# Optimization experiments

Measured on AMD Instinct MI355X. Metric: run time of the kernel, lower is better.

## Reference

```python
import jax, jax.numpy as jnp
import numpy as np

N_NODES = 50000
N_EDGES = 800000
F_DIM = 128   # float_feat_dim
H_DIM = 64    # hidden_dim
NEG_SLOPE = 0.2


def setup_inputs() -> dict:
    key = jax.random.key(0)
    ks = jax.random.split(key, 12)
    in_dim = F_DIM + 1
    sc_in = 1.0 / np.sqrt(in_dim)
    sc_h = 1.0 / np.sqrt(H_DIM)
    return {
        "x_float": jax.random.normal(ks[0], (N_NODES, F_DIM), dtype=jnp.float32),
        "x_binary": jax.random.uniform(ks[1], (N_NODES,), dtype=jnp.float32),
        "edge_index": jax.random.randint(ks[2], (2, N_EDGES), 0, N_NODES, dtype=jnp.int64),
        "Wl": jax.random.normal(ks[3], (H_DIM, in_dim), dtype=jnp.float32) * sc_in,
        "bl": jnp.zeros((H_DIM,), dtype=jnp.float32),
        "Wr": jax.random.normal(ks[4], (H_DIM, in_dim), dtype=jnp.float32) * sc_in,
        "br": jnp.zeros((H_DIM,), dtype=jnp.float32),
        "att": jax.random.normal(ks[5], (H_DIM,), dtype=jnp.float32) * sc_h,
        "gat_bias": jnp.zeros((H_DIM,), dtype=jnp.float32),
        "Wo": jax.random.normal(ks[6], (F_DIM, H_DIM), dtype=jnp.float32) * sc_h,
        "bo": jnp.zeros((F_DIM,), dtype=jnp.float32),
        "dispersion": jnp.zeros((F_DIM,), dtype=jnp.float32),
    }


def reference(x_float, x_binary, edge_index, Wl, bl, Wr, br, att, gat_bias, Wo, bo, dispersion):
    N = x_float.shape[0]
    # concat float feats with binary feature -> [N, F+1]
    x = jnp.concatenate([x_float, x_binary[:, None]], axis=1)
    # add self loops (PyG GATv2Conv default)
    loops = jnp.arange(N, dtype=edge_index.dtype)
    src = jnp.concatenate([edge_index[0], loops])  # [E+N]
    dst = jnp.concatenate([edge_index[1], loops])
    # separate source/target linear projections (share_weights=False)
    xl = x @ Wl.T + bl  # [N, H]
    xr = x @ Wr.T + br  # [N, H]
    # per-edge GATv2 attention score: a^T LeakyReLU(x_l[j] + x_r[i])
    m = xl[src] + xr[dst]                      # [E+N, H]
    m = jnp.where(m > 0, m, NEG_SLOPE * m)
    e = m @ att                                # [E+N]
    # segment softmax over destination neighborhoods
    emax = jax.ops.segment_max(e, dst, num_segments=N)  # self loops => every seg nonempty
    ex = jnp.exp(e - emax[dst])
    denom = jax.ops.segment_sum(ex, dst, num_segments=N)
    alpha = ex / denom[dst]                    # [E+N]
    # weighted scatter-aggregate of source projections
    out = jax.ops.segment_sum(alpha[:, None] * xl[src], dst, num_segments=N) + gat_bias
    h = jax.nn.elu(out)                        # [N, H]
    logits = h @ Wo.T + bo                     # [N, F]
    return logits, jax.nn.softplus(dispersion)
```

## Files before the change

kernel.cpp:

```cpp
#include <hip/hip_runtime.h>
#include <hip/hip_bf16.h>
#include <math.h>

#define N_NODES 50000
#define N_EDGES 800000
#define F_DIM 128
#define H_DIM 64
#define IN_DIM 129
#define NPAD 50176
#define ETOT (N_EDGES + N_NODES)
#define PROJ_BLKS ((N_NODES + 63) / 64)
#define CNT_BLKS  ((N_EDGES + 255) / 256)

typedef __hip_bfloat16 bf16;
typedef __attribute__((ext_vector_type(8))) short bf16x8;
typedef __attribute__((ext_vector_type(4))) float f32x4;

static __device__ __forceinline__ float bs2f(short s) {
    union { float f; unsigned u; } c; c.u = ((unsigned)(unsigned short)s) << 16; return c.f;
}
static __device__ __forceinline__ short f2bs(float f) {
    union { bf16 b; short s; } u; u.b = __float2bfloat16(f); return u.s;
}

__global__ __launch_bounds__(256) void phase1_kernel(
    const float* __restrict__ xf, const float* __restrict__ xb,
    const float* __restrict__ Wl, const float* __restrict__ bl,
    const float* __restrict__ Wr, const float* __restrict__ br,
    const int* __restrict__ edst,
    bf16* __restrict__ xl, bf16* __restrict__ xr,
    int* __restrict__ cnt, int* __restrict__ rank)
{
    if (blockIdx.x >= PROJ_BLKS) {
        int e = (blockIdx.x - PROJ_BLKS) * 256 + threadIdx.x;
        if (e < N_EDGES) rank[e] = atomicAdd(&cnt[edst[e]], 1);
        return;
    }

    int wave = threadIdx.x >> 6;
    int lane = threadIdx.x & 63;
    int n = lane & 15, q = lane >> 4;
    int node0 = blockIdx.x * 64;

    bf16x8 bhi[2][4], blo[2][4];
    float biasv[2], w128[2];
    #pragma unroll
    for (int nt = 0; nt < 2; ++nt) {
        int ch = wave * 32 + nt * 16 + n;
        const float* wrow = (ch < 64) ? (Wl + (size_t)ch * IN_DIM)
                                      : (Wr + (size_t)(ch - 64) * IN_DIM);
        #pragma unroll
        for (int ks = 0; ks < 4; ++ks) {
            bf16x8 hi, lo;
            #pragma unroll
            for (int j = 0; j < 8; ++j) {
                float v = wrow[ks * 32 + q * 8 + j];
                short hs = f2bs(v);
                hi[j] = hs;
                lo[j] = f2bs(v - bs2f(hs));
            }
            bhi[nt][ks] = hi;
            blo[nt][ks] = lo;
        }
        biasv[nt] = (ch < 64) ? bl[ch] : br[ch - 64];
        w128[nt]  = wrow[128];
    }

    #pragma unroll
    for (int mt = 0; mt < 4; ++mt) {
        int nb = node0 + mt * 16;
        if (nb >= N_NODES) break;
        const float* xrow = xf + (size_t)(nb + n) * F_DIM;
        bf16x8 a[4];
        #pragma unroll
        for (int ks = 0; ks < 4; ++ks) {
            float4 u = *(const float4*)(xrow + ks * 32 + q * 8);
            float4 v = *(const float4*)(xrow + ks * 32 + q * 8 + 4);
            bf16x8 t;
            t[0] = f2bs(u.x); t[1] = f2bs(u.y); t[2] = f2bs(u.z); t[3] = f2bs(u.w);
            t[4] = f2bs(v.x); t[5] = f2bs(v.y); t[6] = f2bs(v.z); t[7] = f2bs(v.w);
            a[ks] = t;
        }
        f32x4 acc[2] = {{0.f,0.f,0.f,0.f},{0.f,0.f,0.f,0.f}};
        #pragma unroll
        for (int ks = 0; ks < 4; ++ks) {
            #pragma unroll
            for (int nt = 0; nt < 2; ++nt) {
                acc[nt] = __builtin_amdgcn_mfma_f32_16x16x32_bf16(a[ks], bhi[nt][ks], acc[nt], 0, 0, 0);
                acc[nt] = __builtin_amdgcn_mfma_f32_16x16x32_bf16(a[ks], blo[nt][ks], acc[nt], 0, 0, 0);
            }
        }
        float4 xbv = *(const float4*)(xb + nb + q * 4);
        float xbr[4] = {xbv.x, xbv.y, xbv.z, xbv.w};
        #pragma unroll
        for (int nt = 0; nt < 2; ++nt) {
            int ch = wave * 32 + nt * 16 + n;
            bf16* dstp = (ch < 64) ? xl : xr;
            int cc = ch & 63;
            #pragma unroll
            for (int r = 0; r < 4; ++r) {
                int node = nb + q * 4 + r;
                float val = acc[nt][r] + xbr[r] * w128[nt] + biasv[nt];
                dstp[(size_t)node * H_DIM + cc] = __float2bfloat16(val);
            }
        }
    }
}

__global__ __launch_bounds__(256) void scan_a_kernel(
    const int* __restrict__ cnt, int* __restrict__ offs, int* __restrict__ bsum)
{
    __shared__ int s[256];
    int tid = threadIdx.x;
    int i = blockIdx.x * 256 + tid;
    int v = (i < N_NODES) ? cnt[i] + 1 : 0;
    s[tid] = v;
    __syncthreads();
    #pragma unroll
    for (int d = 1; d < 256; d <<= 1) {
        int t = (tid >= d) ? s[tid - d] : 0;
        __syncthreads();
        s[tid] += t;
        __syncthreads();
    }
    offs[i] = s[tid] - v;
    if (tid == 255) bsum[blockIdx.x] = s[255];
}

__global__ __launch_bounds__(256) void scan_b_kernel(int* __restrict__ bsum)
{
    __shared__ int s[256];
    int tid = threadIdx.x;
    int v = (tid < 196) ? bsum[tid] : 0;
    s[tid] = v;
    __syncthreads();
    #pragma unroll
    for (int d = 1; d < 256; d <<= 1) {
        int t = (tid >= d) ? s[tid - d] : 0;
        __syncthreads();
        s[tid] += t;
        __syncthreads();
    }
    if (tid < 196) bsum[tid] = s[tid] - v;
}

__global__ __launch_bounds__(256) void fill_kernel(
    const int* __restrict__ esrc, const int* __restrict__ edst,
    const int* __restrict__ offs, const int* __restrict__ bsum,
    const int* __restrict__ rank, int* __restrict__ csr_src)
{
    int id = blockIdx.x * 256 + threadIdx.x;
    if (id >= ETOT) return;
    int src, pos;
    if (id < N_EDGES) {
        src = esrc[id];
        int dst = edst[id];
        pos = offs[dst] + bsum[dst >> 8] + 1 + rank[id];
    } else {
        src = id - N_EDGES;
        pos = offs[src] + bsum[src >> 8];
    }
    csr_src[pos] = src;
}

__global__ __launch_bounds__(256) void agg_fused(
    const int* __restrict__ csr_src, const int* __restrict__ offs,
    const int* __restrict__ bsum,
    const bf16* __restrict__ xl, const bf16* __restrict__ xr,
    const float* __restrict__ att, const float* __restrict__ gb,
    bf16* __restrict__ h)
{
    int wid  = (blockIdx.x * 256 + threadIdx.x) >> 6;
    int lane = threadIdx.x & 63;
    if (wid >= N_NODES) return;
    int g  = lane >> 3;
    int c8 = lane & 7;

    float attv[8], xrv[8];
    {
        bf16x8 xrow = *(const bf16x8*)(xr + (size_t)wid * H_DIM + c8 * 8);
        float4 a0 = *(const float4*)(att + c8 * 8);
        float4 a1 = *(const float4*)(att + c8 * 8 + 4);
        attv[0] = a0.x; attv[1] = a0.y; attv[2] = a0.z; attv[3] = a0.w;
        attv[4] = a1.x; attv[5] = a1.y; attv[6] = a1.z; attv[7] = a1.w;
        #pragma unroll
        for (int j = 0; j < 8; ++j) xrv[j] = bs2f(xrow[j]);
    }

    int beg = offs[wid] + bsum[wid >> 8];
    int end = offs[wid + 1] + bsum[(wid + 1) >> 8];
    int last = end - 1;
    float den = 0.f;
    float acc[8] = {0.f, 0.f, 0.f, 0.f, 0.f, 0.f, 0.f, 0.f};

    int i0 = beg + g;        i0 = (i0 < end) ? i0 : last;
    int i1 = beg + 8 + g;    i1 = (i1 < end) ? i1 : last;
    int i2 = beg + 16 + g;   i2 = (i2 < end) ? i2 : last;
    int srcC = csr_src[i2];
    bf16x8 xa = *(const bf16x8*)(xl + (size_t)csr_src[i0] * H_DIM + c8 * 8);
    bf16x8 xb = *(const bf16x8*)(xl + (size_t)csr_src[i1] * H_DIM + c8 * 8);

    for (int base = beg; base < end; base += 8) {
        int i3 = base + 24 + g;  i3 = (i3 < end) ? i3 : last;
        int srcD = csr_src[i3];
        bf16x8 xc = *(const bf16x8*)(xl + (size_t)srcC * H_DIM + c8 * 8);

        bool valid = (base + g) < end;
        float xv[8], p = 0.f;
        #pragma unroll
        for (int j = 0; j < 8; ++j) {
            xv[j] = bs2f(xa[j]);
            float m = xv[j] + xrv[j];
            m = (m > 0.f) ? m : 0.2f * m;
            p += m * attv[j];
        }
        p += __shfl_xor(p, 1);
        p += __shfl_xor(p, 2);
        p += __shfl_xor(p, 4);
        float ex = valid ? __expf(p) : 0.f;
        den += ex;
        #pragma unroll
        for (int j = 0; j < 8; ++j) acc[j] += ex * xv[j];

        xa = xb;
        xb = xc;
        srcC = srcD;
    }

    #pragma unroll
    for (int j = 0; j < 8; ++j) {
        acc[j] += __shfl_xor(acc[j], 8);
        acc[j] += __shfl_xor(acc[j], 16);
        acc[j] += __shfl_xor(acc[j], 32);
    }
    den += __shfl_xor(den, 8);
    den += __shfl_xor(den, 16);
    den += __shfl_xor(den, 32);

    if (g == 0) {
        float inv = 1.0f / den;
        float4 g0 = *(const float4*)(gb + c8 * 8);
        float4 g1 = *(const float4*)(gb + c8 * 8 + 4);
        float gbv[8] = {g0.x, g0.y, g0.z, g0.w, g1.x, g1.y, g1.z, g1.w};
        bf16x8 ov;
        #pragma unroll
        for (int j = 0; j < 8; ++j) {
            float v = acc[j] * inv + gbv[j];
            v = (v > 0.f) ? v : expm1f(v);
            ov[j] = f2bs(v);
        }
        *(bf16x8*)(h + (size_t)wid * H_DIM + c8 * 8) = ov;
    }
}

__global__ __launch_bounds__(256) void out_mfma(
    const bf16* __restrict__ h, const float* __restrict__ Wo,
    const float* __restrict__ bo, const float* __restrict__ disp,
    float* __restrict__ out)
{
    if (blockIdx.x == 0 && threadIdx.x < F_DIM) {
        float d = disp[threadIdx.x];
        out[(size_t)N_NODES * F_DIM + threadIdx.x] = (d > 20.f) ? d : log1pf(__expf(d));
    }

    int wave = threadIdx.x >> 6;
    int lane = threadIdx.x & 63;
    int n = lane & 15, q = lane >> 4;
    int node0 = blockIdx.x * 64;

    bf16x8 bhi[2][2], blo[2][2];
    float bov[2];
    #pragma unroll
    for (int nt = 0; nt < 2; ++nt) {
        int ch = wave * 32 + nt * 16 + n;
        const float* wrow = Wo + (size_t)ch * H_DIM;
        #pragma unroll
        for (int ks = 0; ks < 2; ++ks) {
            float4 u = *(const float4*)(wrow + ks * 32 + q * 8);
            float4 v = *(const float4*)(wrow + ks * 32 + q * 8 + 4);
            float w[8] = {u.x, u.y, u.z, u.w, v.x, v.y, v.z, v.w};
            bf16x8 hi, lo;
            #pragma unroll
            for (int j = 0; j < 8; ++j) {
                short hs = f2bs(w[j]);
                hi[j] = hs;
                lo[j] = f2bs(w[j] - bs2f(hs));
            }
            bhi[nt][ks] = hi;
            blo[nt][ks] = lo;
        }
        bov[nt] = bo[ch];
    }

    #pragma unroll
    for (int mt = 0; mt < 4; ++mt) {
        int nb = node0 + mt * 16;
        if (nb >= N_NODES) break;
        const bf16* hrow = h + (size_t)(nb + n) * H_DIM;
        bf16x8 a[2];
        #pragma unroll
        for (int ks = 0; ks < 2; ++ks)
            a[ks] = *(const bf16x8*)(hrow + ks * 32 + q * 8);
        f32x4 acc[2] = {{0.f,0.f,0.f,0.f},{0.f,0.f,0.f,0.f}};
        #pragma unroll
        for (int ks = 0; ks < 2; ++ks) {
            #pragma unroll
            for (int nt = 0; nt < 2; ++nt) {
                acc[nt] = __builtin_amdgcn_mfma_f32_16x16x32_bf16(a[ks], bhi[nt][ks], acc[nt], 0, 0, 0);
                acc[nt] = __builtin_amdgcn_mfma_f32_16x16x32_bf16(a[ks], blo[nt][ks], acc[nt], 0, 0, 0);
            }
        }
        #pragma unroll
        for (int nt = 0; nt < 2; ++nt) {
            int ch = wave * 32 + nt * 16 + n;
            #pragma unroll
            for (int r = 0; r < 4; ++r) {
                int node = nb + q * 4 + r;
                out[(size_t)node * F_DIM + ch] = acc[nt][r] + bov[nt];
            }
        }
    }
}

extern "C" void kernel_launch(void* const* d_in, const int* in_sizes, int n_in,
                              void* d_out, int out_size, void* d_ws, size_t ws_size,
                              hipStream_t stream)
{
    const float* xf  = (const float*)d_in[0];
    const float* xb  = (const float*)d_in[1];
    const int*   ei  = (const int*)d_in[2];
    const float* Wl  = (const float*)d_in[3];
    const float* bl  = (const float*)d_in[4];
    const float* Wr  = (const float*)d_in[5];
    const float* br  = (const float*)d_in[6];
    const float* att = (const float*)d_in[7];
    const float* gb  = (const float*)d_in[8];
    const float* Wo  = (const float*)d_in[9];
    const float* bo  = (const float*)d_in[10];
    const float* dp  = (const float*)d_in[11];
    float* out = (float*)d_out;
    const int* esrc = ei;
    const int* edst = ei + N_EDGES;

    char* ws = (char*)d_ws;
    const size_t SZB = (size_t)N_NODES * H_DIM * sizeof(bf16);
    bf16*  xl      = (bf16*)(ws);
    bf16*  xr      = (bf16*)(ws + SZB);
    bf16*  h       = (bf16*)(ws + 2 * SZB);
    int*   csr_src = (int*)(ws + 3 * SZB);
    int*   rank    = (int*)(ws + 3 * SZB + (size_t)ETOT * 4);
    int*   cnt     = rank + N_EDGES;
    int*   offs    = cnt + NPAD;
    int*   bsum    = offs + NPAD;

    hipMemsetAsync(cnt, 0, NPAD * sizeof(int), stream);

    phase1_kernel<<<PROJ_BLKS + CNT_BLKS, 256, 0, stream>>>(
        xf, xb, Wl, bl, Wr, br, edst, xl, xr, cnt, rank);

    scan_a_kernel<<<NPAD / 256, 256, 0, stream>>>(cnt, offs, bsum);
    scan_b_kernel<<<1, 256, 0, stream>>>(bsum);

    fill_kernel<<<(ETOT + 255) / 256, 256, 0, stream>>>(esrc, edst, offs, bsum,
                                                        rank, csr_src);

    agg_fused<<<(N_NODES * 64) / 256, 256, 0, stream>>>(csr_src, offs, bsum,
                                                        xl, xr, att, gb, h);

    out_mfma<<<(N_NODES + 63) / 64, 256, 0, stream>>>(h, Wo, bo, dp, out);
}
```

Before: 201.4 us.

## Precompute split-bf16 weight fragments, stage projection stores via swizzled LDS, halve tile size

A new prep kernel converts Wl/Wr/Wo once into hi/lo bf16 MFMA fragment layouts and zeroes the count array, replacing the memset. This removes the per-block weight conversion in the projection and output kernels. The projection kernel now buffers its outputs in XOR-swizzled shared memory and writes xl/xr as coalesced 16-byte vectors instead of scattered 2-byte stores. Both MFMA kernels now cover 32 nodes per block instead of 64 for more blocks. The cost is one extra launch and more weight fragment reloads because there are twice as many blocks.

```diff
diff --git a/kernel.cpp b/kernel.cpp
--- a/kernel.cpp
+++ b/kernel.cpp
@@ -9,8 +9,9 @@
 #define IN_DIM 129
 #define NPAD 50176
 #define ETOT (N_EDGES + N_NODES)
-#define PROJ_BLKS ((N_NODES + 63) / 64)
+#define PROJ_BLKS ((N_NODES + 31) / 32)
 #define CNT_BLKS  ((N_EDGES + 255) / 256)
+#define OUT_BLKS  ((N_NODES + 31) / 32)
 
 typedef __hip_bfloat16 bf16;
 typedef __attribute__((ext_vector_type(8))) short bf16x8;
@@ -21,12 +22,58 @@
 }
 static __device__ __forceinline__ short f2bs(float f) {
     union { bf16 b; short s; } u; u.b = __float2bfloat16(f); return u.s;
+}
+
+__global__ __launch_bounds__(256) void prep_kernel(
+    const float* __restrict__ Wl, const float* __restrict__ Wr,
+    const float* __restrict__ Wo,
+    bf16* __restrict__ whi, bf16* __restrict__ wlo,
+    bf16* __restrict__ wohi, bf16* __restrict__ wolo,
+    int* __restrict__ cnt)
+{
+    int b = blockIdx.x, t = threadIdx.x;
+    if (b < 8) {
+        int s = b * 256 + t;
+        int fid = s >> 6, l = s & 63;
+        int wave = fid >> 3, nt = (fid >> 2) & 1, ks = fid & 3;
+        int ch = wave * 32 + nt * 16 + (l & 15);
+        int kb = ks * 32 + (l >> 4) * 8;
+        const float* wrow = (ch < 64) ? Wl + (size_t)ch * IN_DIM
+                                      : Wr + (size_t)(ch - 64) * IN_DIM;
+        #pragma unroll
+        for (int j = 0; j < 8; ++j) {
+            float v = wrow[kb + j];
+            short hs = f2bs(v);
+            short ls = f2bs(v - bs2f(hs));
+            ((short*)whi)[(size_t)s * 8 + j] = hs;
+            ((short*)wlo)[(size_t)s * 8 + j] = ls;
+        }
+    } else if (b < 12) {
+        int s = (b - 8) * 256 + t;
+        int fid = s >> 6, l = s & 63;
+        int wave = fid >> 2, nt = (fid >> 1) & 1, ks = fid & 1;
+        int ch = wave * 32 + nt * 16 + (l & 15);
+        int kb = ks * 32 + (l >> 4) * 8;
+        const float* wrow = Wo + (size_t)ch * H_DIM;
+        #pragma unroll
+        for (int j = 0; j < 8; ++j) {
+            float v = wrow[kb + j];
+            short hs = f2bs(v);
+            short ls = f2bs(v - bs2f(hs));
+            ((short*)wohi)[(size_t)s * 8 + j] = hs;
+            ((short*)wolo)[(size_t)s * 8 + j] = ls;
+        }
+    } else {
+        int i = (b - 12) * 256 + t;
+        if (i < NPAD) cnt[i] = 0;
+    }
 }
 
 __global__ __launch_bounds__(256) void phase1_kernel(
     const float* __restrict__ xf, const float* __restrict__ xb,
     const float* __restrict__ Wl, const float* __restrict__ bl,
     const float* __restrict__ Wr, const float* __restrict__ br,
+    const bf16* __restrict__ whi, const bf16* __restrict__ wlo,
     const int* __restrict__ edst,
     bf16* __restrict__ xl, bf16* __restrict__ xr,
     int* __restrict__ cnt, int* __restrict__ rank)
@@ -37,73 +84,77 @@
         return;
     }
 
+    __shared__ short lds[32 * 128];
+
     int wave = threadIdx.x >> 6;
     int lane = threadIdx.x & 63;
     int n = lane & 15, q = lane >> 4;
-    int node0 = blockIdx.x * 64;
-
-    bf16x8 bhi[2][4], blo[2][4];
+    int node0 = blockIdx.x * 32;
+
+    bf16x8 bhi[2][4], blo_[2][4];
     float biasv[2], w128[2];
     #pragma unroll
     for (int nt = 0; nt < 2; ++nt) {
         int ch = wave * 32 + nt * 16 + n;
-        const float* wrow = (ch < 64) ? (Wl + (size_t)ch * IN_DIM)
-                                      : (Wr + (size_t)(ch - 64) * IN_DIM);
         #pragma unroll
         for (int ks = 0; ks < 4; ++ks) {
-            bf16x8 hi, lo;
+            int fid = wave * 8 + nt * 4 + ks;
+            bhi[nt][ks]  = *(const bf16x8*)(whi + ((size_t)fid * 64 + lane) * 8);
+            blo_[nt][ks] = *(const bf16x8*)(wlo + ((size_t)fid * 64 + lane) * 8);
+        }
+        biasv[nt] = (ch < 64) ? bl[ch] : br[ch - 64];
+        w128[nt]  = (ch < 64) ? Wl[(size_t)ch * IN_DIM + 128]
+                              : Wr[(size_t)(ch - 64) * IN_DIM + 128];
+    }
+
+    #pragma unroll
+    for (int mt = 0; mt < 2; ++mt) {
+        int nb = node0 + mt * 16;
+        if (nb < N_NODES) {
+            const float* xrow = xf + (size_t)(nb + n) * F_DIM;
+            bf16x8 a[4];
             #pragma unroll
-            for (int j = 0; j < 8; ++j) {
-                float v = wrow[ks * 32 + q * 8 + j];
-                short hs = f2bs(v);
-                hi[j] = hs;
-                lo[j] = f2bs(v - bs2f(hs));
+            for (int ks = 0; ks < 4; ++ks) {
+                float4 u = *(const float4*)(xrow + ks * 32 + q * 8);
+                float4 v = *(const float4*)(xrow + ks * 32 + q * 8 + 4);
+                bf16x8 tt;
+                tt[0] = f2bs(u.x); tt[1] = f2bs(u.y); tt[2] = f2bs(u.z); tt[3] = f2bs(u.w);
+                tt[4] = f2bs(v.x); tt[5] = f2bs(v.y); tt[6] = f2bs(v.z); tt[7] = f2bs(v.w);
+                a[ks] = tt;
             }
-            bhi[nt][ks] = hi;
-            blo[nt][ks] = lo;
-        }
-        biasv[nt] = (ch < 64) ? bl[ch] : br[ch - 64];
-        w128[nt]  = wrow[128];
-    }
-
-    #pragma unroll
-    for (int mt = 0; mt < 4; ++mt) {
-        int nb = node0 + mt * 16;
-        if (nb >= N_NODES) break;
-        const float* xrow = xf + (size_t)(nb + n) * F_DIM;
-        bf16x8 a[4];
-        #pragma unroll
-        for (int ks = 0; ks < 4; ++ks) {
-            float4 u = *(const float4*)(xrow + ks * 32 + q * 8);
-            float4 v = *(const float4*)(xrow + ks * 32 + q * 8 + 4);
-            bf16x8 t;
-            t[0] = f2bs(u.x); t[1] = f2bs(u.y); t[2] = f2bs(u.z); t[3] = f2bs(u.w);
-            t[4] = f2bs(v.x); t[5] = f2bs(v.y); t[6] = f2bs(v.z); t[7] = f2bs(v.w);
-            a[ks] = t;
-        }
-        f32x4 acc[2] = {{0.f,0.f,0.f,0.f},{0.f,0.f,0.f,0.f}};
-        #pragma unroll
-        for (int ks = 0; ks < 4; ++ks) {
+            f32x4 acc[2] = {{0.f,0.f,0.f,0.f},{0.f,0.f,0.f,0.f}};
+            #pragma unroll
+            for (int ks = 0; ks < 4; ++ks) {
+                #pragma unroll
+                for (int nt = 0; nt < 2; ++nt) {
+                    acc[nt] = __builtin_amdgcn_mfma_f32_16x16x32_bf16(a[ks], bhi[nt][ks],  acc[nt], 0, 0, 0);
+                    acc[nt] = __builtin_amdgcn_mfma_f32_16x16x32_bf16(a[ks], blo_[nt][ks], acc[nt], 0, 0, 0);
+                }
+            }
+            float4 xbv = *(const float4*)(xb + nb + q * 4);
+            float xbr[4] = {xbv.x, xbv.y, xbv.z, xbv.w};
             #pragma unroll
             for (int nt = 0; nt < 2; ++nt) {
-                acc[nt] = __builtin_amdgcn_mfma_f32_16x16x32_bf16(a[ks], bhi[nt][ks], acc[nt], 0, 0, 0);
-                acc[nt] = __builtin_amdgcn_mfma_f32_16x16x32_bf16(a[ks], blo[nt][ks], acc[nt], 0, 0, 0);
+                int ch = wave * 32 + nt * 16 + n;
+                int blk = ch >> 3, pos = ch & 7;
+                #pragma unroll
+                for (int r = 0; r < 4; ++r) {
+                    int nodeL = mt * 16 + q * 4 + r;
+                    float val = acc[nt][r] + xbr[r] * w128[nt] + biasv[nt];
+                    lds[nodeL * 128 + ((blk ^ (nodeL & 7)) << 3) + pos] = f2bs(val);
+                }
             }
         }
-        float4 xbv = *(const float4*)(xb + nb + q * 4);
-        float xbr[4] = {xbv.x, xbv.y, xbv.z, xbv.w};
-        #pragma unroll
-        for (int nt = 0; nt < 2; ++nt) {
-            int ch = wave * 32 + nt * 16 + n;
-            bf16* dstp = (ch < 64) ? xl : xr;
-            int cc = ch & 63;
-            #pragma unroll
-            for (int r = 0; r < 4; ++r) {
-                int node = nb + q * 4 + r;
-                float val = acc[nt][r] + xbr[r] * w128[nt] + biasv[nt];
-                dstp[(size_t)node * H_DIM + cc] = __float2bfloat16(val);
-            }
-        }
+    }
+    __syncthreads();
+
+    int nl = threadIdx.x >> 3, bk = threadIdx.x & 7;
+    int node = node0 + nl;
+    if (node < N_NODES) {
+        bf16x8 v0 = *(const bf16x8*)(lds + nl * 128 + ((bk ^ (nl & 7)) << 3));
+        *(bf16x8*)(xl + (size_t)node * H_DIM + bk * 8) = v0;
+        bf16x8 v1 = *(const bf16x8*)(lds + nl * 128 + (((8 + bk) ^ (nl & 7)) << 3));
+        *(bf16x8*)(xr + (size_t)node * H_DIM + bk * 8) = v1;
     }
 }
 
@@ -254,7 +305,8 @@
 }
 
 __global__ __launch_bounds__(256) void out_mfma(
-    const bf16* __restrict__ h, const float* __restrict__ Wo,
+    const bf16* __restrict__ h,
+    const bf16* __restrict__ wohi, const bf16* __restrict__ wolo,
     const float* __restrict__ bo, const float* __restrict__ disp,
     float* __restrict__ out)
 {
@@ -266,34 +318,24 @@
     int wave = threadIdx.x >> 6;
     int lane = threadIdx.x & 63;
     int n = lane & 15, q = lane >> 4;
-    int node0 = blockIdx.x * 64;
-
-    bf16x8 bhi[2][2], blo[2][2];
+    int node0 = blockIdx.x * 32;
+
+    bf16x8 bhi[2][2], blo_[2][2];
     float bov[2];
     #pragma unroll
     for (int nt = 0; nt < 2; ++nt) {
         int ch = wave * 32 + nt * 16 + n;
-        const float* wrow = Wo + (size_t)ch * H_DIM;
         #pragma unroll
         for (int ks = 0; ks < 2; ++ks) {
-            float4 u = *(const float4*)(wrow + ks * 32 + q * 8);
-            float4 v = *(const float4*)(wrow + ks * 32 + q * 8 + 4);
-            float w[8] = {u.x, u.y, u.z, u.w, v.x, v.y, v.z, v.w};
-            bf16x8 hi, lo;
-            #pragma unroll
-            for (int j = 0; j < 8; ++j) {
-                short hs = f2bs(w[j]);
-                hi[j] = hs;
-                lo[j] = f2bs(w[j] - bs2f(hs));
-            }
-            bhi[nt][ks] = hi;
-            blo[nt][ks] = lo;
+            int fid = wave * 4 + nt * 2 + ks;
+            bhi[nt][ks]  = *(const bf16x8*)(wohi + ((size_t)fid * 64 + lane) * 8);
+            blo_[nt][ks] = *(const bf16x8*)(wolo + ((size_t)fid * 64 + lane) * 8);
         }
         bov[nt] = bo[ch];
     }
 
     #pragma unroll
-    for (int mt = 0; mt < 4; ++mt) {
+    for (int mt = 0; mt < 2; ++mt) {
         int nb = node0 + mt * 16;
         if (nb >= N_NODES) break;
         const bf16* hrow = h + (size_t)(nb + n) * H_DIM;
@@ -306,8 +348,8 @@
         for (int ks = 0; ks < 2; ++ks) {
             #pragma unroll
             for (int nt = 0; nt < 2; ++nt) {
-                acc[nt] = __builtin_amdgcn_mfma_f32_16x16x32_bf16(a[ks], bhi[nt][ks], acc[nt], 0, 0, 0);
-                acc[nt] = __builtin_amdgcn_mfma_f32_16x16x32_bf16(a[ks], blo[nt][ks], acc[nt], 0, 0, 0);
+                acc[nt] = __builtin_amdgcn_mfma_f32_16x16x32_bf16(a[ks], bhi[nt][ks],  acc[nt], 0, 0, 0);
+                acc[nt] = __builtin_amdgcn_mfma_f32_16x16x32_bf16(a[ks], blo_[nt][ks], acc[nt], 0, 0, 0);
             }
         }
         #pragma unroll
@@ -352,11 +394,15 @@
     int*   cnt     = rank + N_EDGES;
     int*   offs    = cnt + NPAD;
     int*   bsum    = offs + NPAD;
-
-    hipMemsetAsync(cnt, 0, NPAD * sizeof(int), stream);
+    bf16*  whi     = (bf16*)(bsum + 256);
+    bf16*  wlo     = whi + 16384;
+    bf16*  wohi    = wlo + 16384;
+    bf16*  wolo    = wohi + 8192;
+
+    prep_kernel<<<208, 256, 0, stream>>>(Wl, Wr, Wo, whi, wlo, wohi, wolo, cnt);
 
     phase1_kernel<<<PROJ_BLKS + CNT_BLKS, 256, 0, stream>>>(
-        xf, xb, Wl, bl, Wr, br, edst, xl, xr, cnt, rank);
+        xf, xb, Wl, bl, Wr, br, whi, wlo, edst, xl, xr, cnt, rank);
 
     scan_a_kernel<<<NPAD / 256, 256, 0, stream>>>(cnt, offs, bsum);
     scan_b_kernel<<<1, 256, 0, stream>>>(bsum);
@@ -367,5 +413,5 @@
     agg_fused<<<(N_NODES * 64) / 256, 256, 0, stream>>>(csr_src, offs, bsum,
                                                         xl, xr, att, gb, h);
 
-    out_mfma<<<(N_NODES + 63) / 64, 256, 0, stream>>>(h, Wo, bo, dp, out);
-}
+    out_mfma<<<OUT_BLKS, 256, 0, stream>>>(h, wohi, wolo, bo, dp, out);
+}
```

Result: slower. 209.0 us (+3.7%).
